# Kernel optimization log

Measured on AMD Instinct MI355X. Metric: run time of the kernel, lower is better.

Reference implementation:

```python
import jax, jax.numpy as jnp
import numpy as np

B, LC, LQ, H = 64, 1024, 128, 512
NEG = -1e30


def setup_inputs() -> dict:
    key = jax.random.key(0)
    ks = jax.random.split(key, 12)
    s = 1.0 / np.sqrt(H)
    return {
        "c": jax.random.normal(ks[0], (B, LC, H), jnp.float32),
        "q": jax.random.normal(ks[1], (B, LQ, H), jnp.float32),
        "c_mask": jax.random.randint(ks[2], (B, LC), 0, 2, jnp.int32),
        "q_mask": jax.random.randint(ks[3], (B, LQ), 0, 2, jnp.int32),
        "c_weight": jax.random.normal(ks[4], (H, 1), jnp.float32) * s,
        "q_weight": jax.random.normal(ks[5], (H, 1), jnp.float32) * s,
        "cq_weight": jax.random.normal(ks[6], (1, 1, H), jnp.float32) * s,
        "bias": jnp.zeros((1,), jnp.float32),
        "W1": jax.random.normal(ks[7], (H, H), jnp.float32) * s,
        "b1": jnp.zeros((H,), jnp.float32),
        "W2": jax.random.normal(ks[8], (H, H), jnp.float32) * s,
        "b2": jnp.zeros((H,), jnp.float32),
    }


def reference(c, q, c_mask, q_mask, c_weight, q_weight, cq_weight, bias, W1, b1, W2, b2):
    # --- trilinear similarity (BiDAF eq. 1, memory-efficient form) ---
    s0 = c @ c_weight                                   # [B, LC, 1]
    s1 = jnp.swapaxes(q @ q_weight, 1, 2)               # [B, 1, LQ]
    s2 = jnp.einsum('bch,bqh->bcq', c * cq_weight, q)   # [B, LC, LQ]
    sim = s0 + s1 + s2 + bias

    qm = (q_mask != 0)[:, None, :]   # [B, 1, LQ]
    cm = (c_mask != 0)[:, :, None]   # [B, LC, 1]

    # dual masked softmax (dropout is identity in eval mode)
    s1s = jax.nn.softmax(jnp.where(qm, sim, NEG), axis=2)  # c2q weights
    s2s = jax.nn.softmax(jnp.where(cm, sim, NEG), axis=1)  # q2c weights

    a = s1s @ q                                            # [B, LC, H]
    b = jnp.einsum('bcq,bkq->bck', s1s, s2s) @ c           # [B, LC, H]

    # co-attention branch: qprime = relu(lin2(relu(lin1(q))))
    qp = jax.nn.relu(jax.nn.relu(q @ W1 + b1) @ W2 + b2)   # [B, LQ, H]
    scoat = jnp.einsum('bch,bqh->bcq', c, qp)              # [B, LC, LQ]
    sc1 = jax.nn.softmax(jnp.where(qm, scoat, NEG), axis=2)
    sc2 = jax.nn.softmax(jnp.where(cm, scoat, NEG), axis=1)
    acoat = sc1 @ qp                                       # [B, LC, H]
    bcoat = jnp.einsum('bcq,bch->bqh', sc2, c)             # [B, LQ, H]
    scoat3 = sc1 @ bcoat                                   # [B, LC, H]

    return jnp.concatenate([c, a, c * a, c * b, scoat3, acoat], axis=2)  # [B, LC, 6H]
```

## Files before the change

kernel.cpp:

```cpp
#include <hip/hip_runtime.h>
#include <cstdint>
#include <cstddef>

typedef short  bf16x8 __attribute__((ext_vector_type(8)));
typedef float  f32x4  __attribute__((ext_vector_type(4)));

#define NEGV (-1e30f)
#define LDT 40

__device__ __forceinline__ short f2bf(float x){
    union { float f; unsigned u; } v; v.f = x;
    return (short)((v.u + 0x7fffu + ((v.u >> 16) & 1u)) >> 16);
}
__device__ __forceinline__ float bf2f(short h){
    union { float f; unsigned u; } v; v.u = ((unsigned)(unsigned short)h) << 16; return v.f;
}
__device__ __forceinline__ unsigned packbf(float a, float b){
    return (unsigned)(unsigned short)f2bf(a) | ((unsigned)(unsigned short)f2bf(b) << 16);
}

__global__ __launch_bounds__(256)
void k_prep_w(const float* __restrict__ W1, const float* __restrict__ W2,
              short* __restrict__ W1Th, short* __restrict__ W1Tl,
              short* __restrict__ W2Th, short* __restrict__ W2Tl)
{
    int idx = blockIdx.x * 256 + threadIdx.x;
    int w = idx >> 18;
    int e = idx & ((1 << 18) - 1);
    int n = e & 511, k = e >> 9;
    const float* W = w ? W2 : W1;
    float x = W[k * 512 + n];
    short hi = f2bf(x);
    short lo = f2bf(x - bf2f(hi));
    size_t o = (size_t)n * 512 + k;
    if (w) { W2Th[o] = hi; W2Tl[o] = lo; } else { W1Th[o] = hi; W1Tl[o] = lo; }
}

__global__ __launch_bounds__(256)
void k_prep_q(const float* __restrict__ q, const float* __restrict__ qwv,
              const float* __restrict__ cqw, short* __restrict__ q_cq,
              short* __restrict__ qT, float* __restrict__ s1p)
{
    __shared__ short TT[128 * 136];
    __shared__ float qws[128], cqs[128];
    const int t = threadIdx.x;
    const int b = (int)(blockIdx.x >> 2), hb = (int)(blockIdx.x & 3), h0 = hb * 128;
    if (t < 128) { qws[t] = qwv[h0 + t]; cqs[t] = cqw[h0 + t]; }
    __syncthreads();
    #pragma unroll
    for (int it = 0; it < 16; it++) {
        int idx = it * 256 + t;
        int m = idx >> 5, c4 = (idx & 31) * 4;
        float4 v = *(const float4*)(q + ((size_t)b * 128 + m) * 512 + h0 + c4);
        TT[(c4 + 0) * 136 + m] = f2bf(v.x);
        TT[(c4 + 1) * 136 + m] = f2bf(v.y);
        TT[(c4 + 2) * 136 + m] = f2bf(v.z);
        TT[(c4 + 3) * 136 + m] = f2bf(v.w);
        uint2 d;
        d.x = packbf(v.x * cqs[c4],     v.y * cqs[c4 + 1]);
        d.y = packbf(v.z * cqs[c4 + 2], v.w * cqs[c4 + 3]);
        *(uint2*)(q_cq + ((size_t)b * 128 + m) * 512 + h0 + c4) = d;
        float dot = v.x * qws[c4] + v.y * qws[c4 + 1] + v.z * qws[c4 + 2] + v.w * qws[c4 + 3];
        #pragma unroll
        for (int off = 1; off < 32; off <<= 1) dot += __shfl_xor(dot, off);
        if ((t & 31) == 0) s1p[((size_t)b * 4 + hb) * 128 + m] = dot;
    }
    __syncthreads();
    const int h = t >> 1, half = t & 1;
    short* dst = qT + ((size_t)b * 512 + h0 + h) * 128 + half * 64;
    #pragma unroll
    for (int j = 0; j < 8; j++)
        *(bf16x8*)(dst + j * 8) = *(const bf16x8*)&TT[h * 136 + half * 64 + j * 8];
}

template<bool WT>
__global__ __launch_bounds__(256)
void k_linear(const float* __restrict__ X, const short* __restrict__ WTh,
              const short* __restrict__ WTl, const float* __restrict__ bias,
              float* __restrict__ Y, short* __restrict__ Yh,
              short* __restrict__ Yl, short* __restrict__ YT)
{
    __shared__ __align__(16) short SMEM[4 * 128 * LDT];
    short* Ah = SMEM;
    short* Al = SMEM + 128 * LDT;
    short* Bh = SMEM + 2 * 128 * LDT;
    short* Bl = SMEM + 3 * 128 * LDT;
    const int t = threadIdx.x;
    const int m0 = (int)(blockIdx.x >> 2) * 128;
    const int n0 = (int)(blockIdx.x & 3) * 128;
    const int lane = t & 63;
    const int wr = (t >> 7) & 1, wc = (t >> 6) & 1;
    const int fr = lane & 15, fg = lane >> 4;
    const int srow = t >> 1, sk = (t & 1) * 16;

    f32x4 acc[4][4] = {};

    for (int k0 = 0; k0 < 512; k0 += 32) {
        __syncthreads();
        {
            const float* src = X + (size_t)(m0 + srow) * 512 + k0 + sk;
            float4 f[4];
            #pragma unroll
            for (int i = 0; i < 4; i++) f[i] = ((const float4*)src)[i];
            const float* fv = (const float*)f;
            short hi[16], lo[16];
            #pragma unroll
            for (int j = 0; j < 16; j++) {
                float x = fv[j];
                short h = f2bf(x);
                hi[j] = h; lo[j] = f2bf(x - bf2f(h));
            }
            #pragma unroll
            for (int j = 0; j < 2; j++) {
                *(bf16x8*)&Ah[srow * LDT + sk + j * 8] = *(bf16x8*)&hi[j * 8];
                *(bf16x8*)&Al[srow * LDT + sk + j * 8] = *(bf16x8*)&lo[j * 8];
            }
        }
        {
            const short* sh = WTh + (size_t)(n0 + srow) * 512 + k0 + sk;
            const short* sl = WTl + (size_t)(n0 + srow) * 512 + k0 + sk;
            #pragma unroll
            for (int j = 0; j < 2; j++) {
                *(bf16x8*)&Bh[srow * LDT + sk + j * 8] = ((const bf16x8*)sh)[j];
                *(bf16x8*)&Bl[srow * LDT + sk + j * 8] = ((const bf16x8*)sl)[j];
            }
        }
        __syncthreads();
        bf16x8 a_h[4], a_l[4], b_h[4], b_l[4];
        #pragma unroll
        for (int i = 0; i < 4; i++) {
            int ar = (wr * 64 + i * 16 + fr) * LDT + fg * 8;
            int br = (wc * 64 + i * 16 + fr) * LDT + fg * 8;
            a_h[i] = *(const bf16x8*)&Ah[ar];
            a_l[i] = *(const bf16x8*)&Al[ar];
            b_h[i] = *(const bf16x8*)&Bh[br];
            b_l[i] = *(const bf16x8*)&Bl[br];
        }
        #pragma unroll
        for (int mi = 0; mi < 4; mi++)
        #pragma unroll
        for (int ni = 0; ni < 4; ni++) {
            acc[mi][ni] = __builtin_amdgcn_mfma_f32_16x16x32_bf16(a_h[mi], b_h[ni], acc[mi][ni], 0, 0, 0);
            acc[mi][ni] = __builtin_amdgcn_mfma_f32_16x16x32_bf16(a_h[mi], b_l[ni], acc[mi][ni], 0, 0, 0);
            acc[mi][ni] = __builtin_amdgcn_mfma_f32_16x16x32_bf16(a_l[mi], b_h[ni], acc[mi][ni], 0, 0, 0);
        }
    }
    float bv[4];
    #pragma unroll
    for (int ni = 0; ni < 4; ni++) bv[ni] = bias[n0 + wc * 64 + ni * 16 + fr];

    if (!WT) {
        #pragma unroll
        for (int mi = 0; mi < 4; mi++)
        #pragma unroll
        for (int r = 0; r < 4; r++) {
            int row = m0 + wr * 64 + mi * 16 + fg * 4 + r;
            #pragma unroll
            for (int ni = 0; ni < 4; ni++)
                Y[(size_t)row * 512 + n0 + wc * 64 + ni * 16 + fr] =
                    fmaxf(acc[mi][ni][r] + bv[ni], 0.f);
        }
    } else {
        #pragma unroll
        for (int mi = 0; mi < 4; mi++)
        #pragma unroll
        for (int r = 0; r < 4; r++) {
            int row = m0 + wr * 64 + mi * 16 + fg * 4 + r;
            #pragma unroll
            for (int ni = 0; ni < 4; ni++) {
                float v = fmaxf(acc[mi][ni][r] + bv[ni], 0.f);
                short h = f2bf(v);
                size_t o = (size_t)row * 512 + n0 + wc * 64 + ni * 16 + fr;
                Yh[o] = h;
                Yl[o] = f2bf(v - bf2f(h));
            }
        }
        __syncthreads();
        short* TT = SMEM;
        #pragma unroll
        for (int mi = 0; mi < 4; mi++)
        #pragma unroll
        for (int r = 0; r < 4; r++) {
            int ml = wr * 64 + mi * 16 + fg * 4 + r;
            #pragma unroll
            for (int ni = 0; ni < 4; ni++)
                TT[(wc * 64 + ni * 16 + fr) * 136 + ml] =
                    f2bf(fmaxf(acc[mi][ni][r] + bv[ni], 0.f));
        }
        __syncthreads();
        const int n = t >> 1, half = t & 1;
        short* dst = YT + ((size_t)(m0 >> 7) * 512 + n0 + n) * 128 + half * 64;
        #pragma unroll
        for (int j = 0; j < 8; j++)
            *(bf16x8*)(dst + j * 8) = *(const bf16x8*)&TT[n * 136 + half * 64 + j * 8];
    }
}

template<bool SPLIT, bool ADDS>
__global__ __launch_bounds__(256)
void k_att(const float* __restrict__ Cc, const short* __restrict__ Bhg,
           const short* __restrict__ Blg, const float* __restrict__ cwv,
           const float* __restrict__ s1pg, const float* __restrict__ biasp,
           const int* __restrict__ qmask, const int* __restrict__ cmask,
           short* __restrict__ Pr, short* __restrict__ Pe,
           float2* __restrict__ colpart)
{
    __shared__ __align__(16) short SM[4 * 128 * LDT];
    short* Ah = SM;
    short* Al = SM + 128 * LDT;
    short* Bh = SM + 2 * 128 * LDT;
    short* Bl = SM + 3 * 128 * LDT;
    short* TT = SM;
    __shared__ float red[2][128];
    __shared__ float mrowL[128], rinvL[128], cmaxL[128];
    __shared__ float cws[ADDS ? 512 : 1];
    __shared__ float s0red[ADDS ? 128 : 1][2];
    __shared__ float s0L[ADDS ? 128 : 1], s1L[ADDS ? 128 : 1];
    __shared__ int qmsL[128], cmsL[128];

    const int t = threadIdx.x;
    const int b  = (int)(blockIdx.x & 63);
    const int ch = (int)(blockIdx.x >> 6);
    const int m0 = ch * 128;
    const int lane = t & 63;
    const int wr = (t >> 7) & 1, wc = (t >> 6) & 1;
    const int fr = lane & 15, fg = lane >> 4;
    const int srow = t >> 1, sk = (t & 1) * 16;

    if (ADDS) { cws[t] = cwv[t]; cws[t + 256] = cwv[t + 256]; }
    if (t < 128) {
        qmsL[t] = qmask[b * 128 + t];
        cmsL[t] = cmask[b * 1024 + m0 + t];
        if (ADDS)
            s1L[t] = s1pg[((size_t)b * 4 + 0) * 128 + t] + s1pg[((size_t)b * 4 + 1) * 128 + t]
                   + s1pg[((size_t)b * 4 + 2) * 128 + t] + s1pg[((size_t)b * 4 + 3) * 128 + t];
    }

    const size_t aoff = ((size_t)b * 1024 + m0 + srow) * 512;
    const size_t boff = ((size_t)b * 128 + srow) * 512;
    float s0part = 0.f;
    f32x4 acc[4][4] = {};

    for (int k0 = 0; k0 < 512; k0 += 32) {
        __syncthreads();
        {
            const float* src = Cc + aoff + k0 + sk;
            float4 f[4];
            #pragma unroll
            for (int i = 0; i < 4; i++) f[i] = ((const float4*)src)[i];
            const float* fv = (const float*)f;
            short hi[16], lo[16];
            #pragma unroll
            for (int j = 0; j < 16; j++) {
                float x = fv[j];
                if (ADDS) s0part += x * cws[k0 + sk + j];
                short h = f2bf(x);
                hi[j] = h;
                if (SPLIT) lo[j] = f2bf(x - bf2f(h));
            }
            #pragma unroll
            for (int j = 0; j < 2; j++) {
                *(bf16x8*)&Ah[srow * LDT + sk + j * 8] = *(bf16x8*)&hi[j * 8];
                if (SPLIT) *(bf16x8*)&Al[srow * LDT + sk + j * 8] = *(bf16x8*)&lo[j * 8];
            }
        }
        {
            *(uint4*)&Bh[srow * LDT + sk]     = *(const uint4*)(Bhg + boff + k0 + sk);
            *(uint4*)&Bh[srow * LDT + sk + 8] = *(const uint4*)(Bhg + boff + k0 + sk + 8);
            if (SPLIT) {
                *(uint4*)&Bl[srow * LDT + sk]     = *(const uint4*)(Blg + boff + k0 + sk);
                *(uint4*)&Bl[srow * LDT + sk + 8] = *(const uint4*)(Blg + boff + k0 + sk + 8);
            }
        }
        __syncthreads();
        bf16x8 a_h[4], b_h[4], a_l[4], b_l[4];
        #pragma unroll
        for (int i = 0; i < 4; i++) {
            int ar = (wr * 64 + i * 16 + fr) * LDT + fg * 8;
            int br = (wc * 64 + i * 16 + fr) * LDT + fg * 8;
            a_h[i] = *(const bf16x8*)&Ah[ar];
            b_h[i] = *(const bf16x8*)&Bh[br];
            if (SPLIT) { a_l[i] = *(const bf16x8*)&Al[ar]; b_l[i] = *(const bf16x8*)&Bl[br]; }
        }
        #pragma unroll
        for (int mi = 0; mi < 4; mi++)
        #pragma unroll
        for (int ni = 0; ni < 4; ni++) {
            acc[mi][ni] = __builtin_amdgcn_mfma_f32_16x16x32_bf16(a_h[mi], b_h[ni], acc[mi][ni], 0, 0, 0);
            if (SPLIT) {
                acc[mi][ni] = __builtin_amdgcn_mfma_f32_16x16x32_bf16(a_h[mi], b_l[ni], acc[mi][ni], 0, 0, 0);
                acc[mi][ni] = __builtin_amdgcn_mfma_f32_16x16x32_bf16(a_l[mi], b_h[ni], acc[mi][ni], 0, 0, 0);
            }
        }
    }

    if (ADDS) {
        s0red[srow][t & 1] = s0part;
        __syncthreads();
        if (t < 128) s0L[t] = s0red[t][0] + s0red[t][1];
        __syncthreads();
        float b0 = biasp[0];
        #pragma unroll
        for (int mi = 0; mi < 4; mi++)
        #pragma unroll
        for (int r = 0; r < 4; r++) {
            float s0r = s0L[wr * 64 + mi * 16 + fg * 4 + r] + b0;
            #pragma unroll
            for (int ni = 0; ni < 4; ni++)
                acc[mi][ni][r] += s0r + s1L[wc * 64 + ni * 16 + fr];
        }
    }

    bool qmv[4];
    #pragma unroll
    for (int ni = 0; ni < 4; ni++) qmv[ni] = qmsL[wc * 64 + ni * 16 + fr] != 0;
    bool cmb[4][4];
    #pragma unroll
    for (int mi = 0; mi < 4; mi++)
    #pragma unroll
    for (int r = 0; r < 4; r++) cmb[mi][r] = cmsL[wr * 64 + mi * 16 + fg * 4 + r] != 0;

    #pragma unroll
    for (int mi = 0; mi < 4; mi++)
    #pragma unroll
    for (int r = 0; r < 4; r++) {
        float m = NEGV;
        #pragma unroll
        for (int ni = 0; ni < 4; ni++) if (qmv[ni]) m = fmaxf(m, acc[mi][ni][r]);
        #pragma unroll
        for (int off = 1; off < 16; off <<= 1) m = fmaxf(m, __shfl_xor(m, off));
        if (fr == 0) red[wc][wr * 64 + mi * 16 + fg * 4 + r] = m;
    }
    __syncthreads();
    if (t < 128) mrowL[t] = fmaxf(red[0][t], red[1][t]);
    __syncthreads();
    #pragma unroll
    for (int mi = 0; mi < 4; mi++)
    #pragma unroll
    for (int r = 0; r < 4; r++) {
        float mr = mrowL[wr * 64 + mi * 16 + fg * 4 + r];
        float s = 0.f;
        #pragma unroll
        for (int ni = 0; ni < 4; ni++) if (qmv[ni]) s += __expf(acc[mi][ni][r] - mr);
        #pragma unroll
        for (int off = 1; off < 16; off <<= 1) s += __shfl_xor(s, off);
        if (fr == 0) red[wc][wr * 64 + mi * 16 + fg * 4 + r] = s;
    }
    __syncthreads();
    if (t < 128) rinvL[t] = 1.f / (red[0][t] + red[1][t]);
    __syncthreads();
    #pragma unroll
    for (int mi = 0; mi < 4; mi++)
    #pragma unroll
    for (int r = 0; r < 4; r++) {
        int rowl = wr * 64 + mi * 16 + fg * 4 + r;
        float mr = mrowL[rowl], iv = rinvL[rowl];
        size_t obase = ((size_t)b * 1024 + m0 + rowl) * 128;
        #pragma unroll
        for (int ni = 0; ni < 4; ni++) {
            float o = qmv[ni] ? __expf(acc[mi][ni][r] - mr) * iv : 0.f;
            Pr[obase + wc * 64 + ni * 16 + fr] = f2bf(o);
        }
    }

    float cpart[4];
    #pragma unroll
    for (int ni = 0; ni < 4; ni++) {
        float m = NEGV;
        #pragma unroll
        for (int mi = 0; mi < 4; mi++)
        #pragma unroll
        for (int r = 0; r < 4; r++) if (cmb[mi][r]) m = fmaxf(m, acc[mi][ni][r]);
        m = fmaxf(m, __shfl_xor(m, 16));
        m = fmaxf(m, __shfl_xor(m, 32));
        cpart[ni] = m;
    }
    if (fg == 0) {
        #pragma unroll
        for (int ni = 0; ni < 4; ni++) red[wr][wc * 64 + ni * 16 + fr] = cpart[ni];
    }
    __syncthreads();
    if (t < 128) cmaxL[t] = fmaxf(red[0][t], red[1][t]);
    __syncthreads();
    #pragma unroll
    for (int ni = 0; ni < 4; ni++) {
        const int q = wc * 64 + ni * 16 + fr;
        float cm = cmaxL[q];
        float s = 0.f;
        #pragma unroll
        for (int mi = 0; mi < 4; mi++)
        #pragma unroll
        for (int r = 0; r < 4; r++) {
            int rloc = wr * 64 + mi * 16 + fg * 4 + r;
            float e = cmb[mi][r] ? __expf(acc[mi][ni][r] - cm) : 0.f;
            s += e;
            TT[q * 136 + rloc] = f2bf(e);
        }
        s += __shfl_xor(s, 16);
        s += __shfl_xor(s, 32);
        cpart[ni] = s;
    }
    __syncthreads();
    if (fg == 0) {
        #pragma unroll
        for (int ni = 0; ni < 4; ni++) red[wr][wc * 64 + ni * 16 + fr] = cpart[ni];
    }
    __syncthreads();
    {
        const int q2 = t >> 1, half = t & 1;
        short* dst = Pe + ((size_t)b * 128 + q2) * 1024 + m0 + half * 64;
        #pragma unroll
        for (int j = 0; j < 8; j++)
            *(bf16x8*)(dst + j * 8) = *(const bf16x8*)&TT[q2 * 136 + half * 64 + j * 8];
    }
    if (t < 128) colpart[((size_t)b * 8 + ch) * 128 + t] = make_float2(cmaxL[t], red[0][t] + red[1][t]);
}

__global__ __launch_bounds__(256)
void k_scale(const float2* __restrict__ colpart, short* __restrict__ P)
{
    __shared__ float fL[128];
    const int t = threadIdx.x;
    const int b = (int)(blockIdx.x >> 3), qg = (int)(blockIdx.x & 7);
    if (t < 128) {
        const int q_l = t >> 3, ch = t & 7;
        float2 p = colpart[((size_t)b * 8 + ch) * 128 + qg * 16 + q_l];
        float M = p.x;
        #pragma unroll
        for (int off = 1; off < 8; off <<= 1) M = fmaxf(M, __shfl_xor(M, off));
        float w = p.y * __expf(p.x - M);
        #pragma unroll
        for (int off = 1; off < 8; off <<= 1) w += __shfl_xor(w, off);
        fL[q_l * 8 + ch] = (w > 0.f) ? __expf(p.x - M) / w : 0.f;
    }
    __syncthreads();
    const int q_l = t >> 4, rr = (t & 15) * 64;
    const float f = fL[q_l * 8 + (rr >> 7)];
    short* p = P + ((size_t)b * 128 + qg * 16 + q_l) * 1024 + rr;
    #pragma unroll
    for (int j = 0; j < 8; j++) {
        bf16x8 v = *(bf16x8*)(p + j * 8);
        short o[8];
        #pragma unroll
        for (int l = 0; l < 8; l++) o[l] = f2bf(bf2f(v[l]) * f);
        *(bf16x8*)(p + j * 8) = *(bf16x8*)o;
    }
}

__global__ __launch_bounds__(256)
void k_kgemm2(const short* __restrict__ A1, const short* __restrict__ A2,
              const float* __restrict__ Cc, short* __restrict__ Y1T,
              short* __restrict__ Y2T)
{
    __shared__ __align__(16) short Bs[2][64 * LDT];
    __shared__ __align__(16) short TT[64 * 136];
    const int t = threadIdx.x;
    const int b  = (int)(blockIdx.x & 63);
    const int n0 = (int)(blockIdx.x >> 6) * 64;
    const int lane = t & 63;
    const int w  = t >> 6;
    const int wr = w >> 1, wc = w & 1;
    const int fr = lane & 15, fg = lane >> 4;
    const int n4 = (t & 15) * 4, kk2 = (t >> 4) * 2;

    f32x4 acc1[4][2] = {}, acc2[4][2] = {};

    auto load_e = [&](int k0, float4* e) {
        const float* p = Cc + ((size_t)b * 1024 + k0 + kk2) * 512 + n0 + n4;
        e[0] = *(const float4*)(p);
        e[1] = *(const float4*)(p + 512);
    };
    auto store_b = [&](const float4* e, int buf) {
        const float* p0 = (const float*)&e[0];
        const float* p1 = (const float*)&e[1];
        #pragma unroll
        for (int l = 0; l < 4; l++)
            *(unsigned*)&Bs[buf][(n4 + l) * LDT + kk2] = packbf(p0[l], p1[l]);
    };

    {
        float4 e[2];
        load_e(0, e);
        store_b(e, 0);
    }
    __syncthreads();

    for (int k0 = 0; k0 < 1024; k0 += 32) {
        const int cur = (k0 >> 5) & 1;
        const bool more = (k0 + 32) < 1024;
        float4 e[2];
        if (more) load_e(k0 + 32, e);
        bf16x8 a1[4], a2[4], bg[2];
        #pragma unroll
        for (int i = 0; i < 4; i++) {
            size_t arow = (size_t)(b * 128 + wr * 64 + i * 16 + fr) * 1024 + k0 + fg * 8;
            a1[i] = *(const bf16x8*)(A1 + arow);
            a2[i] = *(const bf16x8*)(A2 + arow);
        }
        #pragma unroll
        for (int i = 0; i < 2; i++)
            bg[i] = *(const bf16x8*)&Bs[cur][(wc * 32 + i * 16 + fr) * LDT + fg * 8];
        #pragma unroll
        for (int mi = 0; mi < 4; mi++)
        #pragma unroll
        for (int ni = 0; ni < 2; ni++) {
            acc1[mi][ni] = __builtin_amdgcn_mfma_f32_16x16x32_bf16(a1[mi], bg[ni], acc1[mi][ni], 0, 0, 0);
            acc2[mi][ni] = __builtin_amdgcn_mfma_f32_16x16x32_bf16(a2[mi], bg[ni], acc2[mi][ni], 0, 0, 0);
        }
        if (more) store_b(e, cur ^ 1);
        __syncthreads();
    }

    const int n_l = t >> 2, qu = t & 3;
    #pragma unroll
    for (int mi = 0; mi < 4; mi++)
    #pragma unroll
    for (int r = 0; r < 4; r++) {
        int ml = wr * 64 + mi * 16 + fg * 4 + r;
        #pragma unroll
        for (int ni = 0; ni < 2; ni++)
            TT[(wc * 32 + ni * 16 + fr) * 136 + ml] = f2bf(acc1[mi][ni][r]);
    }
    __syncthreads();
    {
        short* dst = Y1T + ((size_t)b * 512 + n0 + n_l) * 128 + qu * 32;
        #pragma unroll
        for (int j = 0; j < 4; j++)
            *(bf16x8*)(dst + j * 8) = *(const bf16x8*)&TT[n_l * 136 + qu * 32 + j * 8];
    }
    __syncthreads();
    #pragma unroll
    for (int mi = 0; mi < 4; mi++)
    #pragma unroll
    for (int r = 0; r < 4; r++) {
        int ml = wr * 64 + mi * 16 + fg * 4 + r;
        #pragma unroll
        for (int ni = 0; ni < 2; ni++)
            TT[(wc * 32 + ni * 16 + fr) * 136 + ml] = f2bf(acc2[mi][ni][r]);
    }
    __syncthreads();
    {
        short* dst = Y2T + ((size_t)b * 512 + n0 + n_l) * 128 + qu * 32;
        #pragma unroll
        for (int j = 0; j < 4; j++)
            *(bf16x8*)(dst + j * 8) = *(const bf16x8*)&TT[n_l * 136 + qu * 32 + j * 8];
    }
}

template<bool WITHC>
__global__ __launch_bounds__(256)
void k_epi(const short* __restrict__ Pm, const short* __restrict__ BT1,
           const short* __restrict__ BT2, const float* __restrict__ Cc,
           float* __restrict__ out)
{
    const int t = threadIdx.x;
    const int hb = (int)(blockIdx.x & 3);
    const int mb = (int)((blockIdx.x >> 2) & 7);
    const int b  = (int)(blockIdx.x >> 5);
    const int m0 = mb * 128, h0 = hb * 128;
    const int lane = t & 63;
    const int wr = (t >> 7) & 1, wc = (t >> 6) & 1;
    const int fr = lane & 15, fg = lane >> 4;
    f32x4 acc1[4][4] = {}, acc2[4][4] = {};
    const short* Abase  = Pm  + ((size_t)b * 1024 + m0) * 128;
    const short* B1base = BT1 + ((size_t)b * 512 + h0) * 128;
    const short* B2base = BT2 + ((size_t)b * 512 + h0) * 128;
    #pragma unroll
    for (int kk = 0; kk < 4; kk++) {
        const int k0 = kk * 32;
        bf16x8 af[4], b1[4], b2[4];
        #pragma unroll
        for (int i = 0; i < 4; i++) {
            af[i] = *(const bf16x8*)(Abase  + (size_t)(wr * 64 + i * 16 + fr) * 128 + k0 + fg * 8);
            b1[i] = *(const bf16x8*)(B1base + (size_t)(wc * 64 + i * 16 + fr) * 128 + k0 + fg * 8);
            b2[i] = *(const bf16x8*)(B2base + (size_t)(wc * 64 + i * 16 + fr) * 128 + k0 + fg * 8);
        }
        #pragma unroll
        for (int mi = 0; mi < 4; mi++)
        #pragma unroll
        for (int ni = 0; ni < 4; ni++) {
            acc1[mi][ni] = __builtin_amdgcn_mfma_f32_16x16x32_bf16(af[mi], b1[ni], acc1[mi][ni], 0, 0, 0);
            acc2[mi][ni] = __builtin_amdgcn_mfma_f32_16x16x32_bf16(af[mi], b2[ni], acc2[mi][ni], 0, 0, 0);
        }
    }
    const size_t crow_base = (size_t)b * 1024 + m0;
    #pragma unroll
    for (int mi = 0; mi < 4; mi++)
    #pragma unroll
    for (int r = 0; r < 4; r++) {
        int rowl = wr * 64 + mi * 16 + fg * 4 + r;
        size_t obase = (crow_base + rowl) * 3072 + h0;
        #pragma unroll
        for (int ni = 0; ni < 4; ni++) {
            int col = wc * 64 + ni * 16 + fr;
            float av = acc1[mi][ni][r], bv2 = acc2[mi][ni][r];
            if (WITHC) {
                float cv = Cc[(crow_base + rowl) * 512 + h0 + col];
                out[obase + col]        = cv;
                out[obase + col + 512]  = av;
                out[obase + col + 1024] = cv * av;
                out[obase + col + 1536] = cv * bv2;
            } else {
                out[obase + col + 2048] = bv2;
                out[obase + col + 2560] = av;
            }
        }
    }
}

extern "C" void kernel_launch(void* const* d_in, const int* in_sizes, int n_in,
                              void* d_out, int out_size, void* d_ws, size_t ws_size,
                              hipStream_t stream)
{
    const float* c     = (const float*)d_in[0];
    const float* q     = (const float*)d_in[1];
    const int*   cmask = (const int*)d_in[2];
    const int*   qmask = (const int*)d_in[3];
    const float* cwv   = (const float*)d_in[4];
    const float* qwv   = (const float*)d_in[5];
    const float* cqw   = (const float*)d_in[6];
    const float* bias  = (const float*)d_in[7];
    const float* W1    = (const float*)d_in[8];
    const float* b1    = (const float*)d_in[9];
    const float* W2    = (const float*)d_in[10];
    const float* b2    = (const float*)d_in[11];
    float* out = (float*)d_out;

    char* ws = (char*)d_ws;
    size_t off = 0;
    auto alloc = [&](size_t bytes) -> char* {
        char* p = ws + off;
        off = (off + bytes + 255) & ~(size_t)255;
        return p;
    };
    short* w1th = (short*)alloc(512 * 512 * 2);
    short* w1tl = (short*)alloc(512 * 512 * 2);
    short* w2th = (short*)alloc(512 * 512 * 2);
    short* w2tl = (short*)alloc(512 * 512 * 2);
    float* s1p  = (float*)alloc(64 * 4 * 128 * 4);
    short* q_cq = (short*)alloc((size_t)64 * 128 * 512 * 2);
    short* qT   = (short*)alloc((size_t)64 * 512 * 128 * 2);
    float* z1   = (float*)alloc((size_t)8192 * 512 * 4);
    short* qp_h = (short*)alloc((size_t)8192 * 512 * 2);
    short* qp_l = (short*)alloc((size_t)8192 * 512 * 2);
    short* qpT  = (short*)alloc((size_t)64 * 512 * 128 * 2);
    float2* colpartS = (float2*)alloc((size_t)64 * 8 * 128 * 8);
    float2* colpartC = (float2*)alloc((size_t)64 * 8 * 128 * 8);
    short* s1s  = (short*)alloc((size_t)64 * 1024 * 128 * 2);
    short* s2sT = (short*)alloc((size_t)64 * 128 * 1024 * 2);
    short* sc1  = (short*)alloc((size_t)64 * 1024 * 128 * 2);
    short* sc2T = (short*)alloc((size_t)64 * 128 * 1024 * 2);
    short* binT = (short*)z1;
    short* bcoT = ((short*)z1) + (size_t)64 * 512 * 128;

    k_prep_w<<<2048, 256, 0, stream>>>(W1, W2, w1th, w1tl, w2th, w2tl);
    k_prep_q<<<256, 256, 0, stream>>>(q, qwv, cqw, q_cq, qT, s1p);
    k_linear<false><<<256, 256, 0, stream>>>(q, w1th, w1tl, b1, z1, nullptr, nullptr, nullptr);
    k_linear<true><<<256, 256, 0, stream>>>(z1, w2th, w2tl, b2, nullptr, qp_h, qp_l, qpT);

    k_att<false, true><<<512, 256, 0, stream>>>(
        c, q_cq, nullptr, cwv, s1p, bias, qmask, cmask, s1s, s2sT, colpartS);
    k_scale<<<512, 256, 0, stream>>>(colpartS, s2sT);

    k_att<true, false><<<512, 256, 0, stream>>>(
        c, qp_h, qp_l, nullptr, nullptr, nullptr, qmask, cmask, sc1, sc2T, colpartC);
    k_scale<<<512, 256, 0, stream>>>(colpartC, sc2T);

    k_kgemm2<<<512, 256, 0, stream>>>(s2sT, sc2T, c, binT, bcoT);

    k_epi<true><<<2048, 256, 0, stream>>>(s1s, qT, binT, c, out);
    k_epi<false><<<2048, 256, 0, stream>>>(sc1, qpT, bcoT, nullptr, out);
}
```

Baseline: 671.4 us.

## Permute transposed operand rows for float4 epilogue stores and merge scale launches

The transposed B operands (qT, qpT, binT, bcoT) now have their rows permuted within each 64-column group. This puts the four output columns each lane holds in the epilogue MFMA accumulators next to each other, so the final output writes and the c reads become float4 vector accesses instead of scalar ones. The two k_scale launches are also merged into one 1024-block k_scale2 to save a launch. Correctness depends on the permutation matching the accumulator layout in every producer and consumer.

```diff
diff --git a/kernel.cpp b/kernel.cpp
--- a/kernel.cpp
+++ b/kernel.cpp
@@ -18,6 +18,7 @@
 __device__ __forceinline__ unsigned packbf(float a, float b){
     return (unsigned)(unsigned short)f2bf(a) | ((unsigned)(unsigned short)f2bf(b) << 16);
 }
+__device__ __forceinline__ int p64(int x){ return ((x & 3) << 4) | (x >> 2); }
 
 __global__ __launch_bounds__(256)
 void k_prep_w(const float* __restrict__ W1, const float* __restrict__ W2,
@@ -67,7 +68,8 @@
     }
     __syncthreads();
     const int h = t >> 1, half = t & 1;
-    short* dst = qT + ((size_t)b * 512 + h0 + h) * 128 + half * 64;
+    const int hm = (h & 64) + p64(h & 63);
+    short* dst = qT + ((size_t)b * 512 + h0 + hm) * 128 + half * 64;
     #pragma unroll
     for (int j = 0; j < 8; j++)
         *(bf16x8*)(dst + j * 8) = *(const bf16x8*)&TT[h * 136 + half * 64 + j * 8];
@@ -189,7 +191,8 @@
         }
         __syncthreads();
         const int n = t >> 1, half = t & 1;
-        short* dst = YT + ((size_t)(m0 >> 7) * 512 + n0 + n) * 128 + half * 64;
+        const int nm = (n & 64) + p64(n & 63);
+        short* dst = YT + ((size_t)(m0 >> 7) * 512 + n0 + nm) * 128 + half * 64;
         #pragma unroll
         for (int j = 0; j < 8; j++)
             *(bf16x8*)(dst + j * 8) = *(const bf16x8*)&TT[n * 136 + half * 64 + j * 8];
@@ -417,11 +420,16 @@
 }
 
 __global__ __launch_bounds__(256)
-void k_scale(const float2* __restrict__ colpart, short* __restrict__ P)
+void k_scale2(const float2* __restrict__ cpS, const float2* __restrict__ cpC,
+              short* __restrict__ PS, short* __restrict__ PC)
 {
     __shared__ float fL[128];
+    const int bid = (int)blockIdx.x;
+    const float2* colpart = (bid < 512) ? cpS : cpC;
+    short* P = (bid < 512) ? PS : PC;
+    const int lb = bid & 511;
     const int t = threadIdx.x;
-    const int b = (int)(blockIdx.x >> 3), qg = (int)(blockIdx.x & 7);
+    const int b = lb >> 3, qg = lb & 7;
     if (t < 128) {
         const int q_l = t >> 3, ch = t & 7;
         float2 p = colpart[((size_t)b * 8 + ch) * 128 + qg * 16 + q_l];
@@ -512,6 +520,7 @@
     }
 
     const int n_l = t >> 2, qu = t & 3;
+    const int nm = p64(n_l);
     #pragma unroll
     for (int mi = 0; mi < 4; mi++)
     #pragma unroll
@@ -523,7 +532,7 @@
     }
     __syncthreads();
     {
-        short* dst = Y1T + ((size_t)b * 512 + n0 + n_l) * 128 + qu * 32;
+        short* dst = Y1T + ((size_t)b * 512 + n0 + nm) * 128 + qu * 32;
         #pragma unroll
         for (int j = 0; j < 4; j++)
             *(bf16x8*)(dst + j * 8) = *(const bf16x8*)&TT[n_l * 136 + qu * 32 + j * 8];
@@ -540,7 +549,7 @@
     }
     __syncthreads();
     {
-        short* dst = Y2T + ((size_t)b * 512 + n0 + n_l) * 128 + qu * 32;
+        short* dst = Y2T + ((size_t)b * 512 + n0 + nm) * 128 + qu * 32;
         #pragma unroll
         for (int j = 0; j < 4; j++)
             *(bf16x8*)(dst + j * 8) = *(const bf16x8*)&TT[n_l * 136 + qu * 32 + j * 8];
@@ -584,26 +593,27 @@
         }
     }
     const size_t crow_base = (size_t)b * 1024 + m0;
+    const int colb = wc * 64 + fr * 4;
     #pragma unroll
     for (int mi = 0; mi < 4; mi++)
     #pragma unroll
     for (int r = 0; r < 4; r++) {
         int rowl = wr * 64 + mi * 16 + fg * 4 + r;
-        size_t obase = (crow_base + rowl) * 3072 + h0;
-        #pragma unroll
-        for (int ni = 0; ni < 4; ni++) {
-            int col = wc * 64 + ni * 16 + fr;
-            float av = acc1[mi][ni][r], bv2 = acc2[mi][ni][r];
-            if (WITHC) {
-                float cv = Cc[(crow_base + rowl) * 512 + h0 + col];
-                out[obase + col]        = cv;
-                out[obase + col + 512]  = av;
-                out[obase + col + 1024] = cv * av;
-                out[obase + col + 1536] = cv * bv2;
-            } else {
-                out[obase + col + 2048] = bv2;
-                out[obase + col + 2560] = av;
-            }
+        size_t obase = (crow_base + rowl) * 3072 + h0 + colb;
+        float4 av, bv;
+        av.x = acc1[mi][0][r]; av.y = acc1[mi][1][r]; av.z = acc1[mi][2][r]; av.w = acc1[mi][3][r];
+        bv.x = acc2[mi][0][r]; bv.y = acc2[mi][1][r]; bv.z = acc2[mi][2][r]; bv.w = acc2[mi][3][r];
+        if (WITHC) {
+            float4 cv = *(const float4*)(Cc + (crow_base + rowl) * 512 + h0 + colb);
+            *(float4*)(out + obase) = cv;
+            *(float4*)(out + obase + 512) = av;
+            float4 ca; ca.x = cv.x * av.x; ca.y = cv.y * av.y; ca.z = cv.z * av.z; ca.w = cv.w * av.w;
+            *(float4*)(out + obase + 1024) = ca;
+            float4 cb; cb.x = cv.x * bv.x; cb.y = cv.y * bv.y; cb.z = cv.z * bv.z; cb.w = cv.w * bv.w;
+            *(float4*)(out + obase + 1536) = cb;
+        } else {
+            *(float4*)(out + obase + 2048) = bv;
+            *(float4*)(out + obase + 2560) = av;
         }
     }
 }
@@ -660,11 +670,11 @@
 
     k_att<false, true><<<512, 256, 0, stream>>>(
         c, q_cq, nullptr, cwv, s1p, bias, qmask, cmask, s1s, s2sT, colpartS);
-    k_scale<<<512, 256, 0, stream>>>(colpartS, s2sT);
 
     k_att<true, false><<<512, 256, 0, stream>>>(
         c, qp_h, qp_l, nullptr, nullptr, nullptr, qmask, cmask, sc1, sc2T, colpartC);
-    k_scale<<<512, 256, 0, stream>>>(colpartC, sc2T);
+
+    k_scale2<<<1024, 256, 0, stream>>>(colpartS, colpartC, s2sT, sc2T);
 
     k_kgemm2<<<512, 256, 0, stream>>>(s2sT, sc2T, c, binT, bcoT);
 
```

New measurement: 632.8 us. -5.7%, faster.
